# Kernel optimization log

Measured on AMD Instinct MI355X. Metric: run time of the kernel, lower is better.

## Reference

```python
import jax, jax.numpy as jnp
import numpy as np

C, T, D = 32, 768, 100      # n_countries, n_times, n_ages (=n_features)
H = 5                        # attention heads (EncoderLayer default)
HID_GCN = 60                 # GCN hidden features
FFN = 64                     # feed_forward_dim
NPRED = 10                   # n_predictions
LHID = 200                   # hid_linear_part_dim
NL = 3                       # encoder layers


def setup_inputs() -> dict:
    key = jax.random.key(0)
    ks = jax.random.split(key, 24)
    s = 0.05
    rn = lambda k, shp: jax.random.normal(k, shp, jnp.float32) * s
    return {
        "X": jax.random.normal(ks[0], (C, T, D), jnp.float32),
        "A": jax.random.uniform(ks[1], (C, C), jnp.float32),
        # GCN params
        "gcn_w1": rn(ks[2], (D, HID_GCN)),
        "gcn_b1": rn(ks[3], (HID_GCN,)),
        "gcn_w2": rn(ks[4], (HID_GCN, D)),
        "gcn_b2": rn(ks[5], (D,)),
        # 3 stacked encoder layers
        "enc_wq": rn(ks[6], (NL, H, D, D)),
        "enc_wk": rn(ks[7], (NL, H, D, D)),
        "enc_wv": rn(ks[8], (NL, H, D, D)),
        "enc_wm": rn(ks[9], (NL, H * D, D)),
        "enc_f1w": rn(ks[10], (NL, D, FFN)),
        "enc_f1b": rn(ks[11], (NL, FFN)),
        "enc_f2w": rn(ks[12], (NL, FFN, D)),
        "enc_f2b": rn(ks[13], (NL, D)),
        "enc_ln1g": jnp.ones((NL, D), jnp.float32),
        "enc_ln1b": jnp.zeros((NL, D), jnp.float32),
        "enc_ln2g": jnp.ones((NL, D), jnp.float32),
        "enc_ln2b": jnp.zeros((NL, D), jnp.float32),
        "lin1_w": rn(ks[14], (D, LHID)),
        "lin1_b": rn(ks[15], (LHID,)),
        "lin2_w": rn(ks[16], (LHID, D)),
        "lin2_b": rn(ks[17], (D,)),
    }


def _layer_norm(x, g, b, eps=1e-5):
    m = x.mean(-1, keepdims=True)
    v = ((x - m) ** 2).mean(-1, keepdims=True)
    return (x - m) / jnp.sqrt(v + eps) * g + b


def _encoder_layer(x, wq, wk, wv, wm, f1w, f1b, f2w, f2b, g1, b1, g2, b2):
    # x: [C, T, D]; wq/wk/wv: [H, D, D]
    Q = jnp.einsum('ctd,hde->chte', x, wq)
    K = jnp.einsum('ctd,hde->chte', x, wk)
    V = jnp.einsum('ctd,hde->chte', x, wv)
    scores = jnp.einsum('chte,chse->chts', Q, K) / jnp.sqrt(jnp.float32(D))
    attn = jax.nn.softmax(scores, axis=-1)
    out = jnp.einsum('chts,chse->chte', attn, V)        # [C,H,T,D]
    out = out.transpose(0, 2, 1, 3).reshape(x.shape[0], x.shape[1], H * D)
    x = _layer_norm(x + out @ wm, g1, b1)
    ffn = jax.nn.relu(x @ f1w + f1b) @ f2w + f2b
    return _layer_norm(x + ffn, g2, b2)


def reference(X, A, gcn_w1, gcn_b1, gcn_w2, gcn_b2,
              enc_wq, enc_wk, enc_wv, enc_wm,
              enc_f1w, enc_f1b, enc_f2w, enc_f2b,
              enc_ln1g, enc_ln1b, enc_ln2g, enc_ln2b,
              lin1_w, lin1_b, lin2_w, lin2_b):
    n = A.shape[0]
    adj = A + jnp.eye(n, dtype=A.dtype)
    adj_hat = adj / adj.sum(-1, keepdims=True)
    # GCN layer 1
    h = jnp.einsum('ij,jta->ita', adj_hat, X)
    h = jnp.einsum('ita,ao->ito', h, gcn_w1) + gcn_b1
    h = jax.nn.relu(h)
    # GCN layer 2
    h = jnp.einsum('ij,jta->ita', adj_hat, h)
    h = jnp.einsum('ita,ao->ito', h, gcn_w2) + gcn_b2
    # 3 encoder layers (fixed structural loop)
    for l in range(NL):
        h = _encoder_layer(h, enc_wq[l], enc_wk[l], enc_wv[l], enc_wm[l],
                           enc_f1w[l], enc_f1b[l], enc_f2w[l], enc_f2b[l],
                           enc_ln1g[l], enc_ln1b[l], enc_ln2g[l], enc_ln2b[l])
    last = h[:, -1, :]  # [C, D]
    def step(carry, _):
        p = (carry @ lin1_w + lin1_b) @ lin2_w + lin2_b
        return p, p
    _, preds = jax.lax.scan(step, last, None, length=NPRED)  # [NPRED, C, D]
    return preds.transpose(1, 0, 2)  # [C, NPRED, D]
```

## Files before the change

kernel.cpp:

```cpp
#include <hip/hip_runtime.h>


#define ROWS 24576

#define OFF_ADJ   0L
#define OFF_X0    1024L
#define OFF_X1    (OFF_X0 + 2457600L)
#define OFF_XROW  (OFF_X1 + 3932160L)
#define OFF_XT    (OFF_XROW + 1572864L)
#define OFF_WBF   (OFF_XT + 1572864L)
#define OFF_MHT   (OFF_WBF + 6291456L)
#define OFF_USTT  (OFF_MHT + 122880L)
#define OFF_MP    (OFF_USTT + 98304L)
#define OFF_C0    (OFF_MP + 10000L)
#define OFF_F1WT  (OFF_C0 + 128L)
#define OFF_F2WT  (OFF_F1WT + 12288L)
#define OFF_GW1T  (OFF_F2WT + 10752L)
#define OFF_GW2T  (OFF_GW1T + 4096L)

typedef __attribute__((ext_vector_type(8))) short short8;
typedef __attribute__((ext_vector_type(4))) short short4v;
typedef __attribute__((ext_vector_type(4))) float float4v;
typedef __attribute__((ext_vector_type(2))) unsigned int uint2v;
typedef __attribute__((ext_vector_type(4))) unsigned int uint4v;

__device__ inline unsigned short f2bf(float f) {
    unsigned u = __builtin_bit_cast(unsigned, f);
    return (unsigned short)((u + 0x7fffu + ((u >> 16) & 1u)) >> 16);
}
__device__ inline unsigned pk2bf(float lo, float hi) {
    unsigned r;
    asm("v_cvt_pk_bf16_f32 %0, %1, %2" : "=v"(r) : "v"(lo), "v"(hi));
    return r;
}
__device__ inline void st4s(short* p, unsigned a, unsigned b) {
    *(short4v*)p = __builtin_bit_cast(short4v, (uint2v){a, b});
}
__device__ inline float bf2f(unsigned short v) {
    return __builtin_bit_cast(float, ((unsigned)v) << 16);
}
__device__ inline void gload16(const short* g, short* l) {
    __builtin_amdgcn_global_load_lds((const __attribute__((address_space(1))) void*)g,
                                     (__attribute__((address_space(3))) void*)l, 16, 0, 0);
}
__device__ inline int permt(int t) {
    int tl = t & 63, q = tl >> 2, r = tl & 3;
    int pos = (q & 8) | ((q & 3) << 1) | ((q >> 2) & 1);
    return (t & ~63) | (pos << 2) | r;
}

__global__ void __launch_bounds__(256) k_mu2(const float* __restrict__ wq, const float* __restrict__ wk,
                                             const float* __restrict__ wv, const float* __restrict__ wm,
                                             const float* __restrict__ l1w, const float* __restrict__ l1b,
                                             const float* __restrict__ l2w, const float* __restrict__ l2b,
                                             const float* __restrict__ f1w, const float* __restrict__ f2w,
                                             const float* __restrict__ A,
                                             const float* __restrict__ gw1, const float* __restrict__ gw2,
                                             unsigned short* __restrict__ MhT, unsigned short* __restrict__ UstT,
                                             float* __restrict__ Mp, float* __restrict__ c0v,
                                             unsigned short* __restrict__ f1wT, unsigned short* __restrict__ f2wT,
                                             float* __restrict__ adjh,
                                             unsigned short* __restrict__ gw1T, unsigned short* __restrict__ gw2T) {
    int bi = blockIdx.x, tid = threadIdx.x;
    if (bi < 480) {
        int mat = bi >> 4, sub = bi & 15;
        int mode = mat / 15, idx = mat % 15, l = idx / 5, h = idx % 5;
        const float* Asrc = (mode == 0 ? wq : wv) + (l*5 + h)*10000;
        const float* Bsrc = (mode == 0) ? (wk + (l*5 + h)*10000) : (wm + l*50000 + h*10000);
        int oend = sub*625 + 625;
        for (int o = sub*625 + tid; o < oend; o += 256) {
            int r = o / 100, cix = o - (o/100)*100;
            const float* arow = Asrc + r*100;
            float acc = 0.f;
            if (mode == 0) {
                const float* brow = Bsrc + cix*100;
                float4 s = {0,0,0,0};
                #pragma unroll 5
                for (int e4 = 0; e4 < 25; ++e4) {
                    float4 av = *(const float4*)(arow + e4*4);
                    float4 bv = *(const float4*)(brow + e4*4);
                    s.x += av.x*bv.x; s.y += av.y*bv.y;
                    s.z += av.z*bv.z; s.w += av.w*bv.w;
                }
                acc = (s.x + s.y) + (s.z + s.w);
                MhT[(long)(l*5 + h)*16384 + cix*128 + r] = f2bf(acc * 0.1f);
            } else {
                for (int e = 0; e < 100; ++e) acc += arow[e] * Bsrc[e*100 + cix];
                UstT[(long)l*65536 + (long)cix*512 + h*100 + r] = f2bf(acc);
            }
        }
        if (sub == 0) {
            if (mode == 0) {
                unsigned short* M0 = MhT + (long)(l*5 + h)*16384;
                for (int i = tid; i < 28*128; i += 256) M0[(100 + i/128)*128 + (i%128)] = 0;
                for (int i = tid; i < 100*28; i += 256) M0[(i/28)*128 + 100 + (i%28)] = 0;
            } else if (h == 4) {
                unsigned short* U0 = UstT + (long)l*65536;
                for (int i = tid; i < 28*512; i += 256) U0[(long)(100 + i/512)*512 + (i%512)] = 0;
                for (int i = tid; i < 100*12; i += 256) U0[(long)(i/12)*512 + 500 + (i%12)] = 0;
            }
        }
    } else if (bi < 496) {
        int sub = bi - 480;
        int oend = sub*625 + 625;
        for (int o = sub*625 + tid; o < oend; o += 256) {
            int r = o / 100, cix = o - (o/100)*100;
            const float* arow = l1w + r*200;
            float acc = 0.f;
            for (int e = 0; e < 200; ++e) acc += arow[e] * l2w[e*100 + cix];
            Mp[r*100 + cix] = acc;
        }
    } else if (bi == 496) {
        if (tid < 100) {
            float acc = l2b[tid];
            for (int e = 0; e < 200; ++e) acc += l1b[e] * l2w[e*100 + tid];
            c0v[tid] = acc;
        }
    } else if (bi < 500) {
        int l = bi - 497;
        unsigned short* F1 = f1wT + (long)l*8192;
        for (int i = tid; i < 8192; i += 256) {
            int o = i >> 7, k = i & 127;
            F1[i] = (k < 100) ? f2bf(f1w[l*6400 + k*64 + o]) : (unsigned short)0;
        }
        unsigned short* F2 = f2wT + (long)l*7168;
        for (int i = tid; i < 7168; i += 256) {
            int o2 = i >> 6, k2 = i & 63;
            F2[i] = (o2 < 100) ? f2bf(f2w[l*6400 + k2*100 + o2]) : (unsigned short)0;
        }
    } else if (bi == 500) {
        __shared__ float adj[1024];
        __shared__ float rs[32];
        for (int i = tid; i < 1024; i += 256) {
            int r = i >> 5, j = i & 31;
            adj[i] = A[i] + (r == j ? 1.f : 0.f);
        }
        __syncthreads();
        if (tid < 32) {
            float s = 0.f;
            #pragma unroll
            for (int jj = 0; jj < 32; ++jj) s += adj[tid*32 + jj];
            rs[tid] = s;
        }
        __syncthreads();
        for (int i = tid; i < 1024; i += 256) adjh[i] = adj[i] / rs[i >> 5];
    } else {
        for (int i = tid; i < 8192; i += 256) {
            int o = i >> 7, k = i & 127;
            gw1T[i] = (o < 60 && k < 100) ? f2bf(gw1[k*60 + o]) : (unsigned short)0;
        }
        for (int i = tid; i < 7168; i += 256) {
            int o = i >> 6, k = i & 63;
            gw2T[i] = (o < 100 && k < 60) ? f2bf(gw2[k*100 + o]) : (unsigned short)0;
        }
    }
}

__global__ void __launch_bounds__(128) k_gw1(const float* __restrict__ X,
                                             const unsigned short* __restrict__ gw1T,
                                             unsigned short* __restrict__ g) {
    const int tid = threadIdx.x, wave = tid >> 6, lane = tid & 63;
    const int l15 = lane & 15, l4 = lane >> 4;
    const long row = (long)blockIdx.x*32 + wave*16 + l15;
    const float* xrp = X + row*100;
    float4v acc[4];
    #pragma unroll
    for (int mt = 0; mt < 4; ++mt) acc[mt] = (float4v){0,0,0,0};
    #pragma unroll
    for (int ks = 0; ks < 4; ++ks) {
        const int k0 = ks*32 + l4*8;
        short8 b;
        if (k0 + 8 <= 100) {
            float4 v0 = *(const float4*)(xrp + k0);
            float4 v1 = *(const float4*)(xrp + k0 + 4);
            b[0] = (short)f2bf(v0.x); b[1] = (short)f2bf(v0.y);
            b[2] = (short)f2bf(v0.z); b[3] = (short)f2bf(v0.w);
            b[4] = (short)f2bf(v1.x); b[5] = (short)f2bf(v1.y);
            b[6] = (short)f2bf(v1.z); b[7] = (short)f2bf(v1.w);
        } else if (k0 < 100) {
            float4 v0 = *(const float4*)(xrp + k0);
            b[0] = (short)f2bf(v0.x); b[1] = (short)f2bf(v0.y);
            b[2] = (short)f2bf(v0.z); b[3] = (short)f2bf(v0.w);
            b[4] = 0; b[5] = 0; b[6] = 0; b[7] = 0;
        } else {
            #pragma unroll
            for (int e = 0; e < 8; ++e) b[e] = 0;
        }
        #pragma unroll
        for (int mt = 0; mt < 4; ++mt) {
            short8 a = *(const short8*)((const short*)gw1T + (mt*16 + l15)*128 + ks*32 + l4*8);
            acc[mt] = __builtin_amdgcn_mfma_f32_16x16x32_bf16(a, b, acc[mt], 0, 0, 0);
        }
    }
    #pragma unroll
    for (int mt = 0; mt < 4; ++mt) {
        int o0 = mt*16 + l4*4;
        *(uint2v*)(g + row*64 + o0) =
            (uint2v){pk2bf(acc[mt][0], acc[mt][1]), pk2bf(acc[mt][2], acc[mt][3])};
    }
}

__global__ void __launch_bounds__(256) k_spmmg(const float* __restrict__ adjh,
                                               const unsigned short* __restrict__ g,
                                               const float* __restrict__ b1,
                                               unsigned short* __restrict__ hid) {
    __shared__ float adj[1024];
    int tid = threadIdx.x;
    for (int i = tid; i < 1024; i += 256) adj[i] = adjh[i];
    __syncthreads();
    long p = (long)blockIdx.x*256 + tid;
    int o = (int)(p & 63);
    float acc[32];
    #pragma unroll
    for (int i = 0; i < 32; ++i) acc[i] = 0.f;
    for (int j = 0; j < 32; ++j) {
        float xv = bf2f(g[(long)j*49152 + p]);
        #pragma unroll
        for (int i = 0; i < 32; ++i) acc[i] += adj[i*32 + j] * xv;
    }
    float bias = (o < 60) ? b1[o] : 0.f;
    #pragma unroll
    for (int i = 0; i < 32; ++i) hid[(long)i*49152 + p] = f2bf(fmaxf(acc[i] + bias, 0.f));
}

__global__ void __launch_bounds__(128) k_gw2(const unsigned short* __restrict__ hid,
                                             const unsigned short* __restrict__ gw2T,
                                             unsigned short* __restrict__ h2) {
    const int tid = threadIdx.x, wave = tid >> 6, lane = tid & 63;
    const int l15 = lane & 15, l4 = lane >> 4;
    const long row = (long)blockIdx.x*32 + wave*16 + l15;
    float4v acc[7];
    #pragma unroll
    for (int mt = 0; mt < 7; ++mt) acc[mt] = (float4v){0,0,0,0};
    #pragma unroll
    for (int ks = 0; ks < 2; ++ks) {
        short8 b = *(const short8*)((const short*)hid + row*64 + ks*32 + l4*8);
        #pragma unroll
        for (int mt = 0; mt < 7; ++mt) {
            short8 a = *(const short8*)((const short*)gw2T + (mt*16 + l15)*64 + ks*32 + l4*8);
            acc[mt] = __builtin_amdgcn_mfma_f32_16x16x32_bf16(a, b, acc[mt], 0, 0, 0);
        }
    }
    #pragma unroll
    for (int mt = 0; mt < 7; ++mt) {
        int o0 = mt*16 + l4*4;
        *(uint2v*)(h2 + row*128 + o0) =
            (uint2v){pk2bf(acc[mt][0], acc[mt][1]), pk2bf(acc[mt][2], acc[mt][3])};
    }
    *(uint2v*)(h2 + row*128 + 112 + l4*4) = (uint2v){0u, 0u};
}

__global__ void __launch_bounds__(384) k_spmmx(const float* __restrict__ adjh,
                                               const unsigned short* __restrict__ h2,
                                               const float* __restrict__ b2,
                                               float* __restrict__ x0,
                                               unsigned short* __restrict__ xrow,
                                               unsigned short* __restrict__ xT) {
    __shared__ float adj[1024];
    int tid = threadIdx.x;
    for (int i = tid; i < 1024; i += 384) adj[i] = adjh[i];
    __syncthreads();
    long p = (long)blockIdx.x*384 + tid;
    int o = (int)(p & 127);
    int t = (int)(p >> 7);
    int tp = permt(t);
    float acc[32];
    #pragma unroll
    for (int i = 0; i < 32; ++i) acc[i] = 0.f;
    for (int j = 0; j < 32; ++j) {
        float xv = bf2f(h2[(long)j*98304 + p]);
        #pragma unroll
        for (int i = 0; i < 32; ++i) acc[i] += adj[i*32 + j] * xv;
    }
    if (o < 100) {
        float bias = b2[o];
        #pragma unroll
        for (int i = 0; i < 32; ++i) {
            float v = acc[i] + bias;
            x0[((long)i*768 + t)*100 + o] = v;
            unsigned short bv = f2bf(v);
            xrow[((long)i*768 + t)*128 + o] = bv;
            xT[(long)i*98304 + (long)o*768 + tp] = bv;
        }
    } else {
        #pragma unroll
        for (int i = 0; i < 32; ++i) {
            xrow[((long)i*768 + t)*128 + o] = 0;
            if (o < 112) xT[(long)i*98304 + (long)o*768 + tp] = 0;
        }
    }
}

__global__ void __launch_bounds__(256, 4) k_attn12(const unsigned short* __restrict__ xrow,
                                                   const unsigned short* __restrict__ xT,
                                                   const unsigned short* __restrict__ MhT,
                                                   unsigned short* __restrict__ Wb) {
    __shared__ __align__(16) short xr[2][64 * 128];
    __shared__ __align__(16) short xt[112 * 64];
    const int tid = threadIdx.x;
    const int wave = tid >> 6, lane = tid & 63;
    const int l15 = lane & 15, l4 = lane >> 4;
    const int c = blockIdx.z, h = blockIdx.y, q0 = blockIdx.x * 128;

    const short* xrg = (const short*)xrow + (long)c*768*128;
    const short* xtg = (const short*)xT + (long)c*128*768;
    const int rl4 = lane >> 4, cp16 = lane & 15;
    const int rl8 = lane >> 3, cp8 = lane & 7;
    const int njt = (wave == 3) ? 2 : 4;
    const int sw8 = (l15 & 7) << 3;
    const int swt = l15 & 7;

    #pragma unroll
    for (int j = 0; j < 4; ++j) {
        int row = wave*16 + j*4 + rl4;
        int lc = cp16 ^ (row & 7);
        gload16(xrg + (long)row*128 + lc*8, xr[0] + (wave*16 + j*4)*128);
    }

    short8 qb0[4], qb1[4];
    {
        short* mq = &xr[1][wave * 16 * 128];
        const short* Mb = (const short*)MhT + (long)h*16384 + l15*128 + l4*8;
        const short* xq = (const short*)xrow + ((long)c*768 + q0 + wave*16 + l15)*128 + l4*8;
        short8 bq0[4], bq1[4];
        #pragma unroll
        for (int kk = 0; kk < 4; ++kk) {
            bq0[kk] = *(const short8*)(xq + kk*32);
            bq1[kk] = *(const short8*)(xq + 64*128 + kk*32);
        }
        float4v qc0[8], qc1[8];
        #pragma unroll
        for (int mt = 0; mt < 8; ++mt) { qc0[mt] = (float4v){0,0,0,0}; qc1[mt] = (float4v){0,0,0,0}; }
        __builtin_amdgcn_s_setprio(1);
        #pragma unroll
        for (int mt = 0; mt < 8; ++mt) {
            #pragma unroll
            for (int kk = 0; kk < 4; ++kk) {
                short8 a = *(const short8*)(Mb + (mt*16)*128 + kk*32);
                qc0[mt] = __builtin_amdgcn_mfma_f32_16x16x32_bf16(a, bq0[kk], qc0[mt], 0, 0, 0);
                qc1[mt] = __builtin_amdgcn_mfma_f32_16x16x32_bf16(a, bq1[kk], qc1[mt], 0, 0, 0);
            }
        }
        __builtin_amdgcn_s_setprio(0);
        #pragma unroll
        for (int mt = 0; mt < 8; ++mt)
            st4s(mq + l15*128 + ((mt*16 + l4*4) ^ sw8),
                 pk2bf(qc0[mt][0], qc0[mt][1]), pk2bf(qc0[mt][2], qc0[mt][3]));
        asm volatile("" ::: "memory");
        #pragma unroll
        for (int kk = 0; kk < 4; ++kk)
            qb0[kk] = *(const short8*)(mq + l15*128 + ((kk*32 + l4*8) ^ sw8));
        asm volatile("" ::: "memory");
        #pragma unroll
        for (int mt = 0; mt < 8; ++mt)
            st4s(mq + l15*128 + ((mt*16 + l4*4) ^ sw8),
                 pk2bf(qc1[mt][0], qc1[mt][1]), pk2bf(qc1[mt][2], qc1[mt][3]));
        asm volatile("" ::: "memory");
        #pragma unroll
        for (int kk = 0; kk < 4; ++kk)
            qb1[kk] = *(const short8*)(mq + l15*128 + ((kk*32 + l4*8) ^ sw8));
    }

    __syncthreads();

    float4v o0[7], o1[7];
    #pragma unroll
    for (int n = 0; n < 7; ++n) { o0[n] = (float4v){0,0,0,0}; o1[n] = (float4v){0,0,0,0}; }
    float lsum0 = 0.f, lsum1 = 0.f;

    for (int kt = 0; kt < 12; ++kt) {
        const int key0 = kt * 64;
        const short* xrb = xr[kt & 1];

        for (int j = 0; j < njt; ++j) {
            int row = wave*32 + j*8 + rl8;
            int lc = cp8 ^ (row & 7);
            gload16(xtg + (long)row*768 + key0 + lc*8, xt + (wave*32 + j*8)*64);
        }
        if (kt < 11) {
            short* xrn = xr[(kt + 1) & 1];
            #pragma unroll
            for (int j = 0; j < 4; ++j) {
                int row = wave*16 + j*4 + rl4;
                int lc = cp16 ^ (row & 7);
                gload16(xrg + (long)(key0 + 64 + row)*128 + lc*8, xrn + (wave*16 + j*4)*128);
            }
        }
        __builtin_amdgcn_sched_barrier(0);

        unsigned pw0[4], pw1[4];
        __builtin_amdgcn_s_setprio(1);
        #pragma unroll
        for (int kn = 0; kn < 2; ++kn) {
            float4v s0 = (float4v){0,0,0,0}, s1 = (float4v){0,0,0,0};
            #pragma unroll
            for (int kk = 0; kk < 4; ++kk) {
                short8 a = *(const short8*)(xrb + (kn*16 + l15)*128 + (((kk*4 + l4) ^ (l15 & 7))*8));
                s0 = __builtin_amdgcn_mfma_f32_16x16x32_bf16(a, qb0[kk], s0, 0, 0, 0);
                s1 = __builtin_amdgcn_mfma_f32_16x16x32_bf16(a, qb1[kk], s1, 0, 0, 0);
            }
            float p0[4], p1[4];
            #pragma unroll
            for (int r = 0; r < 4; ++r) {
                p0[r] = __expf(s0[r]); lsum0 += p0[r];
                p1[r] = __expf(s1[r]); lsum1 += p1[r];
            }
            pw0[kn*2]   = pk2bf(p0[0], p0[1]); pw0[kn*2+1] = pk2bf(p0[2], p0[3]);
            pw1[kn*2]   = pk2bf(p1[0], p1[1]); pw1[kn*2+1] = pk2bf(p1[2], p1[3]);
        }
        __builtin_amdgcn_s_setprio(0);

        if (kt < 11) { asm volatile("s_waitcnt vmcnt(4)" ::: "memory"); }
        else         { asm volatile("s_waitcnt vmcnt(0)" ::: "memory"); }
        __builtin_amdgcn_s_barrier();

        __builtin_amdgcn_s_setprio(1);
        {
            short8 b0 = __builtin_bit_cast(short8, (uint4v){pw0[0], pw0[1], pw0[2], pw0[3]});
            short8 b1 = __builtin_bit_cast(short8, (uint4v){pw1[0], pw1[1], pw1[2], pw1[3]});
            const int offA = ((l4 ^ swt) * 8);
            #pragma unroll
            for (int dt = 0; dt < 7; ++dt) {
                short8 a = *(const short8*)(xt + (dt*16 + l15)*64 + offA);
                o0[dt] = __builtin_amdgcn_mfma_f32_16x16x32_bf16(a, b0, o0[dt], 0, 0, 0);
                o1[dt] = __builtin_amdgcn_mfma_f32_16x16x32_bf16(a, b1, o1[dt], 0, 0, 0);
            }
        }

        unsigned pw0b[4], pw1b[4];
        #pragma unroll
        for (int kn = 2; kn < 4; ++kn) {
            float4v s0 = (float4v){0,0,0,0}, s1 = (float4v){0,0,0,0};
            #pragma unroll
            for (int kk = 0; kk < 4; ++kk) {
                short8 a = *(const short8*)(xrb + (kn*16 + l15)*128 + (((kk*4 + l4) ^ (l15 & 7))*8));
                s0 = __builtin_amdgcn_mfma_f32_16x16x32_bf16(a, qb0[kk], s0, 0, 0, 0);
                s1 = __builtin_amdgcn_mfma_f32_16x16x32_bf16(a, qb1[kk], s1, 0, 0, 0);
            }
            float p0[4], p1[4];
            #pragma unroll
            for (int r = 0; r < 4; ++r) {
                p0[r] = __expf(s0[r]); lsum0 += p0[r];
                p1[r] = __expf(s1[r]); lsum1 += p1[r];
            }
            pw0b[(kn-2)*2]   = pk2bf(p0[0], p0[1]); pw0b[(kn-2)*2+1] = pk2bf(p0[2], p0[3]);
            pw1b[(kn-2)*2]   = pk2bf(p1[0], p1[1]); pw1b[(kn-2)*2+1] = pk2bf(p1[2], p1[3]);
        }

        {
            short8 b0 = __builtin_bit_cast(short8, (uint4v){pw0b[0], pw0b[1], pw0b[2], pw0b[3]});
            short8 b1 = __builtin_bit_cast(short8, (uint4v){pw1b[0], pw1b[1], pw1b[2], pw1b[3]});
            const int offB = (((4 + l4) ^ swt) * 8);
            #pragma unroll
            for (int dt = 0; dt < 7; ++dt) {
                short8 a = *(const short8*)(xt + (dt*16 + l15)*64 + offB);
                o0[dt] = __builtin_amdgcn_mfma_f32_16x16x32_bf16(a, b0, o0[dt], 0, 0, 0);
                o1[dt] = __builtin_amdgcn_mfma_f32_16x16x32_bf16(a, b1, o1[dt], 0, 0, 0);
            }
        }
        __builtin_amdgcn_s_setprio(0);
        __syncthreads();
    }

    float l0 = lsum0, l1 = lsum1;
    l0 += __shfl_xor(l0, 16, 64); l0 += __shfl_xor(l0, 32, 64);
    l1 += __shfl_xor(l1, 16, 64); l1 += __shfl_xor(l1, 32, 64);
    float inv0 = 1.f / l0, inv1 = 1.f / l1;

    unsigned short* Wo0 = Wb + ((long)(c*768 + q0 + wave*16 + l15))*512 + h*100 + l4*4;
    unsigned short* Wo1 = Wo0 + 64*512;
    #pragma unroll
    for (int dt = 0; dt < 7; ++dt) {
        if (dt < 6 || l4 == 0) {
            *(uint2v*)(Wo0 + dt*16) = (uint2v){pk2bf(o0[dt][0]*inv0, o0[dt][1]*inv0),
                                               pk2bf(o0[dt][2]*inv0, o0[dt][3]*inv0)};
            *(uint2v*)(Wo1 + dt*16) = (uint2v){pk2bf(o1[dt][0]*inv1, o1[dt][1]*inv1),
                                               pk2bf(o1[dt][2]*inv1, o1[dt][3]*inv1)};
        }
    }
    if (h == 0) {
        unsigned short* Wz = Wb + ((long)c*768 + q0)*512 + 500;
        for (int i = tid; i < 1536; i += 256) Wz[(long)(i/12)*512 + (i%12)] = 0;
    }
}

template<bool EMIT>
__global__ void __launch_bounds__(128) k_tail(const unsigned short* __restrict__ Wb,
        const unsigned short* __restrict__ UstT,
        const unsigned short* __restrict__ f1wT, const unsigned short* __restrict__ f2wT,
        const float* __restrict__ f1b, const float* __restrict__ f2b,
        const float* __restrict__ g1, const float* __restrict__ b1,
        const float* __restrict__ g2, const float* __restrict__ b2,
        float* __restrict__ x, unsigned short* __restrict__ xrow, unsigned short* __restrict__ xT) {
    __shared__ __align__(16) short ust[2][128 * 64];
    const int tid = threadIdx.x, wave = tid >> 6, lane = tid & 63;
    const int l15 = lane & 15, l4 = lane >> 4;
    const long row = (long)blockIdx.x*32 + wave*16 + l15;
    const int cc = blockIdx.x / 24;
    const int tt = (blockIdx.x % 24)*32 + wave*16 + l15;
    const int ttp = permt(tt);
    const int sr8 = lane >> 3, sc8 = lane & 7;

    const short* Wr = (const short*)Wb + row*512 + l4*8;
    float4v o[8];
    #pragma unroll
    for (int mt = 0; mt < 8; ++mt) o[mt] = (float4v){0,0,0,0};

    {
        short* dst = ust[0];
        #pragma unroll
        for (int j = 0; j < 8; ++j) {
            int r = wave*64 + j*8 + sr8;
            int lc = sc8 ^ (r & 7);
            gload16((const short*)UstT + (long)r*512 + 0 + lc*8, dst + (wave*64 + j*8)*64);
        }
    }
    __syncthreads();

    short8 bc0 = *(const short8*)(Wr + 0);
    short8 bc1 = *(const short8*)(Wr + 32);
    for (int cb = 0; cb < 8; ++cb) {
        if (cb < 7) {
            const int ksb = (cb + 1) * 64;
            short* dst = ust[(cb + 1) & 1];
            #pragma unroll
            for (int j = 0; j < 8; ++j) {
                int r = wave*64 + j*8 + sr8;
                int lc = sc8 ^ (r & 7);
                gload16((const short*)UstT + (long)r*512 + ksb + lc*8, dst + (wave*64 + j*8)*64);
            }
        }
        short8 bn0, bn1;
        if (cb < 7) {
            bn0 = *(const short8*)(Wr + (cb*2 + 2)*32);
            bn1 = *(const short8*)(Wr + (cb*2 + 3)*32);
        }
        __builtin_amdgcn_sched_barrier(0);

        const short* bufc = ust[cb & 1];
        __builtin_amdgcn_s_setprio(1);
        #pragma unroll
        for (int mt = 0; mt < 8; ++mt) {
            short8 a0 = *(const short8*)(bufc + (mt*16 + l15)*64 + (((0*4 + l4) ^ (l15 & 7))*8));
            o[mt] = __builtin_amdgcn_mfma_f32_16x16x32_bf16(a0, bc0, o[mt], 0, 0, 0);
            short8 a1 = *(const short8*)(bufc + (mt*16 + l15)*64 + (((1*4 + l4) ^ (l15 & 7))*8));
            o[mt] = __builtin_amdgcn_mfma_f32_16x16x32_bf16(a1, bc1, o[mt], 0, 0, 0);
        }
        __builtin_amdgcn_s_setprio(0);
        bc0 = bn0; bc1 = bn1;
        __syncthreads();
    }

    short* myz = ust[0] + wave * 2176;
    short* myt = ust[1] + wave * 1152;

    float zv[7][4];
    float sum = 0.f;
    #pragma unroll
    for (int mt = 0; mt < 7; ++mt) {
        int f0 = mt*16 + l4*4;
        float4 xv = {0,0,0,0};
        if (f0 < 100) xv = *(const float4*)(x + row*100 + f0);
        #pragma unroll
        for (int r = 0; r < 4; ++r) {
            float z = 0.f;
            if (f0 < 100) { z = o[mt][r] + ((const float*)&xv)[r]; sum += z; }
            zv[mt][r] = z;
        }
    }
    sum += __shfl_xor(sum, 16, 64); sum += __shfl_xor(sum, 32, 64);
    float mean = sum * 0.01f;
    float vs = 0.f;
    #pragma unroll
    for (int mt = 0; mt < 7; ++mt) {
        if (mt*16 + l4*4 < 100) {
            #pragma unroll
            for (int r = 0; r < 4; ++r) { float d = zv[mt][r] - mean; vs += d*d; }
        }
    }
    vs += __shfl_xor(vs, 16, 64); vs += __shfl_xor(vs, 32, 64);
    float inv = rsqrtf(vs * 0.01f + 1e-5f);
    float x1r[7][4];
    #pragma unroll
    for (int mt = 0; mt < 7; ++mt) {
        int f0 = mt*16 + l4*4;
        float4 gv = {0,0,0,0}, bv = {0,0,0,0};
        if (f0 < 100) { gv = *(const float4*)(g1 + f0); bv = *(const float4*)(b1 + f0); }
        #pragma unroll
        for (int r = 0; r < 4; ++r)
            x1r[mt][r] = (f0 < 100) ? (zv[mt][r] - mean) * inv * ((const float*)&gv)[r] + ((const float*)&bv)[r] : 0.f;
    }

    #pragma unroll
    for (int mt = 0; mt < 8; ++mt) {
        float v0 = (mt < 7) ? x1r[mt][0] : 0.f, v1 = (mt < 7) ? x1r[mt][1] : 0.f;
        float v2 = (mt < 7) ? x1r[mt][2] : 0.f, v3 = (mt < 7) ? x1r[mt][3] : 0.f;
        st4s(myz + l15*136 + mt*16 + l4*4, pk2bf(v0, v1), pk2bf(v2, v3));
    }
    asm volatile("" ::: "memory");

    float4v t2[4];
    #pragma unroll
    for (int m2t = 0; m2t < 4; ++m2t) t2[m2t] = (float4v){0,0,0,0};
    #pragma unroll
    for (int ks = 0; ks < 4; ++ks) {
        short8 b = *(const short8*)(myz + l15*136 + ks*32 + l4*8);
        #pragma unroll
        for (int m2t = 0; m2t < 4; ++m2t) {
            short8 a = *(const short8*)((const short*)f1wT + (m2t*16 + l15)*128 + ks*32 + l4*8);
            t2[m2t] = __builtin_amdgcn_mfma_f32_16x16x32_bf16(a, b, t2[m2t], 0, 0, 0);
        }
    }
    #pragma unroll
    for (int m2t = 0; m2t < 4; ++m2t) {
        int m20 = m2t*16 + l4*4;
        float4 bv = *(const float4*)(f1b + m20);
        float v0 = fmaxf(t2[m2t][0] + ((const float*)&bv)[0], 0.f);
        float v1 = fmaxf(t2[m2t][1] + ((const float*)&bv)[1], 0.f);
        float v2 = fmaxf(t2[m2t][2] + ((const float*)&bv)[2], 0.f);
        float v3 = fmaxf(t2[m2t][3] + ((const float*)&bv)[3], 0.f);
        st4s(myt + l15*72 + m20, pk2bf(v0, v1), pk2bf(v2, v3));
    }
    asm volatile("" ::: "memory");

    float4v o3[7];
    #pragma unroll
    for (int m3t = 0; m3t < 7; ++m3t) o3[m3t] = (float4v){0,0,0,0};
    #pragma unroll
    for (int ks2 = 0; ks2 < 2; ++ks2) {
        short8 b = *(const short8*)(myt + l15*72 + ks2*32 + l4*8);
        #pragma unroll
        for (int m3t = 0; m3t < 7; ++m3t) {
            short8 a = *(const short8*)((const short*)f2wT + (m3t*16 + l15)*64 + ks2*32 + l4*8);
            o3[m3t] = __builtin_amdgcn_mfma_f32_16x16x32_bf16(a, b, o3[m3t], 0, 0, 0);
        }
    }

    float z2[7][4];
    float sum2 = 0.f;
    #pragma unroll
    for (int m3t = 0; m3t < 7; ++m3t) {
        int f0 = m3t*16 + l4*4;
        float4 bv = {0,0,0,0};
        if (f0 < 100) bv = *(const float4*)(f2b + f0);
        #pragma unroll
        for (int r = 0; r < 4; ++r) {
            float z = 0.f;
            if (f0 < 100) { z = o3[m3t][r] + ((const float*)&bv)[r] + x1r[m3t][r]; sum2 += z; }
            z2[m3t][r] = z;
        }
    }
    sum2 += __shfl_xor(sum2, 16, 64); sum2 += __shfl_xor(sum2, 32, 64);
    float mean2 = sum2 * 0.01f;
    float vs2 = 0.f;
    #pragma unroll
    for (int m3t = 0; m3t < 7; ++m3t) {
        if (m3t*16 + l4*4 < 100) {
            #pragma unroll
            for (int r = 0; r < 4; ++r) { float d = z2[m3t][r] - mean2; vs2 += d*d; }
        }
    }
    vs2 += __shfl_xor(vs2, 16, 64); vs2 += __shfl_xor(vs2, 32, 64);
    float inv2 = rsqrtf(vs2 * 0.01f + 1e-5f);

    unsigned short* xTc = EMIT ? (xT + (long)cc*98304 + ttp) : nullptr;
    #pragma unroll
    for (int m3t = 0; m3t < 7; ++m3t) {
        int f0 = m3t*16 + l4*4;
        if (f0 < 100) {
            float4 gv = *(const float4*)(g2 + f0);
            float4 bv = *(const float4*)(b2 + f0);
            float y[4];
            #pragma unroll
            for (int r = 0; r < 4; ++r)
                y[r] = (z2[m3t][r] - mean2) * inv2 * ((const float*)&gv)[r] + ((const float*)&bv)[r];
            *(float4*)(x + row*100 + f0) = (float4){y[0], y[1], y[2], y[3]};
            if (EMIT) {
                *(uint2v*)(xrow + row*128 + f0) = (uint2v){pk2bf(y[0], y[1]), pk2bf(y[2], y[3])};
                #pragma unroll
                for (int r = 0; r < 4; ++r)
                    xTc[(long)(f0 + r)*768] = f2bf(y[r]);
            }
        } else if (EMIT) {
            *(uint2v*)(xrow + row*128 + f0) = (uint2v){0u, 0u};
            #pragma unroll
            for (int r = 0; r < 4; ++r)
                if (f0 + r < 112) xTc[(long)(f0 + r)*768] = 0;
        }
    }
    if (EMIT) *(uint2v*)(xrow + row*128 + 112 + l4*4) = (uint2v){0u, 0u};
}

__global__ void __launch_bounds__(256) k_pred2(const float* __restrict__ xf,
        const float* __restrict__ Mp, const float* __restrict__ c0v,
        float* __restrict__ out) {
    int c = blockIdx.x, tid = threadIdx.x;
    __shared__ float Ml[10000];
    __shared__ float carry[100];
    for (int i = tid; i < 10000; i += 256) Ml[i] = Mp[i];
    if (tid < 100) carry[tid] = xf[((long)c*768 + 767)*100 + tid];
    __syncthreads();
    for (int s = 0; s < 10; ++s) {
        float pv = 0.f;
        if (tid < 100) {
            pv = c0v[tid];
            for (int d = 0; d < 100; ++d) pv += carry[d] * Ml[d*100 + tid];
            out[((long)c*10 + s)*100 + tid] = pv;
        }
        __syncthreads();
        if (tid < 100) carry[tid] = pv;
        __syncthreads();
    }
}

extern "C" void kernel_launch(void* const* d_in, const int* in_sizes, int n_in,
                              void* d_out, int out_size, void* d_ws, size_t ws_size,
                              hipStream_t stream) {
    const float* X    = (const float*)d_in[0];
    const float* A    = (const float*)d_in[1];
    const float* gw1  = (const float*)d_in[2];
    const float* gb1  = (const float*)d_in[3];
    const float* gw2  = (const float*)d_in[4];
    const float* gb2  = (const float*)d_in[5];
    const float* wq   = (const float*)d_in[6];
    const float* wk   = (const float*)d_in[7];
    const float* wv   = (const float*)d_in[8];
    const float* wm   = (const float*)d_in[9];
    const float* f1w  = (const float*)d_in[10];
    const float* f1b  = (const float*)d_in[11];
    const float* f2w  = (const float*)d_in[12];
    const float* f2b  = (const float*)d_in[13];
    const float* ln1g = (const float*)d_in[14];
    const float* ln1b = (const float*)d_in[15];
    const float* ln2g = (const float*)d_in[16];
    const float* ln2b = (const float*)d_in[17];
    const float* l1w  = (const float*)d_in[18];
    const float* l1b  = (const float*)d_in[19];
    const float* l2w  = (const float*)d_in[20];
    const float* l2b  = (const float*)d_in[21];
    (void)in_sizes; (void)n_in; (void)out_size; (void)ws_size;

    float* ws   = (float*)d_ws;
    float* adjh = ws + OFF_ADJ;
    float* x0   = ws + OFF_X0;
    unsigned short* gbuf = (unsigned short*)(ws + OFF_X1);
    unsigned short* hbuf = (unsigned short*)(ws + OFF_X1 + 786432L);
    unsigned short* h2buf= (unsigned short*)(ws + OFF_X1 + 1572864L);
    unsigned short* xrow = (unsigned short*)(ws + OFF_XROW);
    unsigned short* xTb  = (unsigned short*)(ws + OFF_XT);
    unsigned short* Wbf  = (unsigned short*)(ws + OFF_WBF);
    unsigned short* MhT  = (unsigned short*)(ws + OFF_MHT);
    unsigned short* UstT = (unsigned short*)(ws + OFF_USTT);
    float* Mp   = ws + OFF_MP;
    float* c0v  = ws + OFF_C0;
    unsigned short* f1wT = (unsigned short*)(ws + OFF_F1WT);
    unsigned short* f2wT = (unsigned short*)(ws + OFF_F2WT);
    unsigned short* gw1T = (unsigned short*)(ws + OFF_GW1T);
    unsigned short* gw2T = (unsigned short*)(ws + OFF_GW2T);
    float* out  = (float*)d_out;

    k_mu2<<<502, 256, 0, stream>>>(wq, wk, wv, wm, l1w, l1b, l2w, l2b, f1w, f2w, A, gw1, gw2,
                                   MhT, UstT, Mp, c0v, f1wT, f2wT, adjh, gw1T, gw2T);

    k_gw1<<<768, 128, 0, stream>>>(X, gw1T, gbuf);
    k_spmmg<<<192, 256, 0, stream>>>(adjh, gbuf, gb1, hbuf);
    k_gw2<<<768, 128, 0, stream>>>(hbuf, gw2T, h2buf);
    k_spmmx<<<256, 384, 0, stream>>>(adjh, h2buf, gb2, x0, xrow, xTb);

    for (int l = 0; l < 3; ++l) {
        k_attn12<<<dim3(6,5,32), 256, 0, stream>>>(xrow, xTb, MhT + (long)l*81920, Wbf);
        if (l < 2)
            k_tail<true><<<768, 128, 0, stream>>>(Wbf, UstT + (long)l*65536,
                f1wT + (long)l*8192, f2wT + (long)l*7168, f1b + l*64, f2b + l*100,
                ln1g + l*100, ln1b + l*100, ln2g + l*100, ln2b + l*100, x0, xrow, xTb);
        else
            k_tail<false><<<768, 128, 0, stream>>>(Wbf, UstT + (long)l*65536,
                f1wT + (long)l*8192, f2wT + (long)l*7168, f1b + l*64, f2b + l*100,
                ln1g + l*100, ln1b + l*100, ln2g + l*100, ln2b + l*100, x0, xrow, xTb);
    }

    k_pred2<<<32, 256, 0, stream>>>(x0, Mp, c0v, out);
}
```

Measured before the change: 461.2 us.

## Split attention query tile across 8 waves with one 16-row tile each

The attention kernel now runs 512 threads (8 waves) per block instead of 256, and each wave handles a single 16-query tile instead of two. Cooperative K/V tile loads are redistributed over the 8 waves, and the vmcnt wait threshold is adjusted to match. Per-wave register pressure and accumulator state roughly halve, which lets more waves hide latency. The cost is that each wave reuses every LDS-loaded key fragment for half as many query tiles, so LDS read traffic per unit of MFMA work doubles.

```diff
diff --git a/kernel.cpp b/kernel.cpp
--- a/kernel.cpp
+++ b/kernel.cpp
@@ -291,10 +291,10 @@
     }
 }
 
-__global__ void __launch_bounds__(256, 4) k_attn12(const unsigned short* __restrict__ xrow,
-                                                   const unsigned short* __restrict__ xT,
-                                                   const unsigned short* __restrict__ MhT,
-                                                   unsigned short* __restrict__ Wb) {
+__global__ void __launch_bounds__(512) k_attn14(const unsigned short* __restrict__ xrow,
+                                                const unsigned short* __restrict__ xT,
+                                                const unsigned short* __restrict__ MhT,
+                                                unsigned short* __restrict__ Wb) {
     __shared__ __align__(16) short xr[2][64 * 128];
     __shared__ __align__(16) short xt[112 * 64];
     const int tid = threadIdx.x;
@@ -306,181 +306,152 @@
     const short* xtg = (const short*)xT + (long)c*128*768;
     const int rl4 = lane >> 4, cp16 = lane & 15;
     const int rl8 = lane >> 3, cp8 = lane & 7;
-    const int njt = (wave == 3) ? 2 : 4;
+    const int njt = (wave < 7) ? 2 : 0;
     const int sw8 = (l15 & 7) << 3;
     const int swt = l15 & 7;
 
-    #pragma unroll
-    for (int j = 0; j < 4; ++j) {
-        int row = wave*16 + j*4 + rl4;
-        int lc = cp16 ^ (row & 7);
-        gload16(xrg + (long)row*128 + lc*8, xr[0] + (wave*16 + j*4)*128);
-    }
-
-    short8 qb0[4], qb1[4];
+    short8 qb[4];
     {
-        short* mq = &xr[1][wave * 16 * 128];
+        short* mq = &xr[0][0] + wave * 2048;
         const short* Mb = (const short*)MhT + (long)h*16384 + l15*128 + l4*8;
         const short* xq = (const short*)xrow + ((long)c*768 + q0 + wave*16 + l15)*128 + l4*8;
-        short8 bq0[4], bq1[4];
-        #pragma unroll
-        for (int kk = 0; kk < 4; ++kk) {
-            bq0[kk] = *(const short8*)(xq + kk*32);
-            bq1[kk] = *(const short8*)(xq + 64*128 + kk*32);
-        }
-        float4v qc0[8], qc1[8];
-        #pragma unroll
-        for (int mt = 0; mt < 8; ++mt) { qc0[mt] = (float4v){0,0,0,0}; qc1[mt] = (float4v){0,0,0,0}; }
+        short8 bq[4];
+        #pragma unroll
+        for (int kk = 0; kk < 4; ++kk) bq[kk] = *(const short8*)(xq + kk*32);
+        float4v qc[8];
+        #pragma unroll
+        for (int mt = 0; mt < 8; ++mt) qc[mt] = (float4v){0,0,0,0};
         __builtin_amdgcn_s_setprio(1);
         #pragma unroll
         for (int mt = 0; mt < 8; ++mt) {
             #pragma unroll
             for (int kk = 0; kk < 4; ++kk) {
                 short8 a = *(const short8*)(Mb + (mt*16)*128 + kk*32);
-                qc0[mt] = __builtin_amdgcn_mfma_f32_16x16x32_bf16(a, bq0[kk], qc0[mt], 0, 0, 0);
-                qc1[mt] = __builtin_amdgcn_mfma_f32_16x16x32_bf16(a, bq1[kk], qc1[mt], 0, 0, 0);
+                qc[mt] = __builtin_amdgcn_mfma_f32_16x16x32_bf16(a, bq[kk], qc[mt], 0, 0, 0);
             }
         }
         __builtin_amdgcn_s_setprio(0);
         #pragma unroll
         for (int mt = 0; mt < 8; ++mt)
             st4s(mq + l15*128 + ((mt*16 + l4*4) ^ sw8),
-                 pk2bf(qc0[mt][0], qc0[mt][1]), pk2bf(qc0[mt][2], qc0[mt][3]));
+                 pk2bf(qc[mt][0], qc[mt][1]), pk2bf(qc[mt][2], qc[mt][3]));
         asm volatile("" ::: "memory");
         #pragma unroll
         for (int kk = 0; kk < 4; ++kk)
-            qb0[kk] = *(const short8*)(mq + l15*128 + ((kk*32 + l4*8) ^ sw8));
+            qb[kk] = *(const short8*)(mq + l15*128 + ((kk*32 + l4*8) ^ sw8));
         asm volatile("" ::: "memory");
-        #pragma unroll
-        for (int mt = 0; mt < 8; ++mt)
-            st4s(mq + l15*128 + ((mt*16 + l4*4) ^ sw8),
-                 pk2bf(qc1[mt][0], qc1[mt][1]), pk2bf(qc1[mt][2], qc1[mt][3]));
-        asm volatile("" ::: "memory");
-        #pragma unroll
-        for (int kk = 0; kk < 4; ++kk)
-            qb1[kk] = *(const short8*)(mq + l15*128 + ((kk*32 + l4*8) ^ sw8));
     }
 
     __syncthreads();
 
-    float4v o0[7], o1[7];
-    #pragma unroll
-    for (int n = 0; n < 7; ++n) { o0[n] = (float4v){0,0,0,0}; o1[n] = (float4v){0,0,0,0}; }
-    float lsum0 = 0.f, lsum1 = 0.f;
+    #pragma unroll
+    for (int j = 0; j < 2; ++j) {
+        int row = wave*8 + j*4 + rl4;
+        int lc = cp16 ^ (row & 7);
+        gload16(xrg + (long)row*128 + lc*8, xr[0] + (wave*8 + j*4)*128);
+    }
+    __syncthreads();
+
+    float4v o[7];
+    #pragma unroll
+    for (int n = 0; n < 7; ++n) o[n] = (float4v){0,0,0,0};
+    float lsum = 0.f;
 
     for (int kt = 0; kt < 12; ++kt) {
         const int key0 = kt * 64;
         const short* xrb = xr[kt & 1];
 
         for (int j = 0; j < njt; ++j) {
-            int row = wave*32 + j*8 + rl8;
+            int row = wave*16 + j*8 + rl8;
             int lc = cp8 ^ (row & 7);
-            gload16(xtg + (long)row*768 + key0 + lc*8, xt + (wave*32 + j*8)*64);
+            gload16(xtg + (long)row*768 + key0 + lc*8, xt + (wave*16 + j*8)*64);
         }
         if (kt < 11) {
             short* xrn = xr[(kt + 1) & 1];
             #pragma unroll
-            for (int j = 0; j < 4; ++j) {
-                int row = wave*16 + j*4 + rl4;
+            for (int j = 0; j < 2; ++j) {
+                int row = wave*8 + j*4 + rl4;
                 int lc = cp16 ^ (row & 7);
-                gload16(xrg + (long)(key0 + 64 + row)*128 + lc*8, xrn + (wave*16 + j*4)*128);
+                gload16(xrg + (long)(key0 + 64 + row)*128 + lc*8, xrn + (wave*8 + j*4)*128);
             }
         }
         __builtin_amdgcn_sched_barrier(0);
 
-        unsigned pw0[4], pw1[4];
+        unsigned pw[4];
         __builtin_amdgcn_s_setprio(1);
         #pragma unroll
         for (int kn = 0; kn < 2; ++kn) {
-            float4v s0 = (float4v){0,0,0,0}, s1 = (float4v){0,0,0,0};
+            float4v s0 = (float4v){0,0,0,0};
             #pragma unroll
             for (int kk = 0; kk < 4; ++kk) {
                 short8 a = *(const short8*)(xrb + (kn*16 + l15)*128 + (((kk*4 + l4) ^ (l15 & 7))*8));
-                s0 = __builtin_amdgcn_mfma_f32_16x16x32_bf16(a, qb0[kk], s0, 0, 0, 0);
-                s1 = __builtin_amdgcn_mfma_f32_16x16x32_bf16(a, qb1[kk], s1, 0, 0, 0);
-            }
-            float p0[4], p1[4];
-            #pragma unroll
-            for (int r = 0; r < 4; ++r) {
-                p0[r] = __expf(s0[r]); lsum0 += p0[r];
-                p1[r] = __expf(s1[r]); lsum1 += p1[r];
-            }
-            pw0[kn*2]   = pk2bf(p0[0], p0[1]); pw0[kn*2+1] = pk2bf(p0[2], p0[3]);
-            pw1[kn*2]   = pk2bf(p1[0], p1[1]); pw1[kn*2+1] = pk2bf(p1[2], p1[3]);
+                s0 = __builtin_amdgcn_mfma_f32_16x16x32_bf16(a, qb[kk], s0, 0, 0, 0);
+            }
+            float p[4];
+            #pragma unroll
+            for (int r = 0; r < 4; ++r) { p[r] = __expf(s0[r]); lsum += p[r]; }
+            pw[kn*2]   = pk2bf(p[0], p[1]); pw[kn*2+1] = pk2bf(p[2], p[3]);
         }
         __builtin_amdgcn_s_setprio(0);
 
-        if (kt < 11) { asm volatile("s_waitcnt vmcnt(4)" ::: "memory"); }
+        if (kt < 11) { asm volatile("s_waitcnt vmcnt(2)" ::: "memory"); }
         else         { asm volatile("s_waitcnt vmcnt(0)" ::: "memory"); }
         __builtin_amdgcn_s_barrier();
 
         __builtin_amdgcn_s_setprio(1);
         {
-            short8 b0 = __builtin_bit_cast(short8, (uint4v){pw0[0], pw0[1], pw0[2], pw0[3]});
-            short8 b1 = __builtin_bit_cast(short8, (uint4v){pw1[0], pw1[1], pw1[2], pw1[3]});
+            short8 b0 = __builtin_bit_cast(short8, (uint4v){pw[0], pw[1], pw[2], pw[3]});
             const int offA = ((l4 ^ swt) * 8);
             #pragma unroll
             for (int dt = 0; dt < 7; ++dt) {
                 short8 a = *(const short8*)(xt + (dt*16 + l15)*64 + offA);
-                o0[dt] = __builtin_amdgcn_mfma_f32_16x16x32_bf16(a, b0, o0[dt], 0, 0, 0);
-                o1[dt] = __builtin_amdgcn_mfma_f32_16x16x32_bf16(a, b1, o1[dt], 0, 0, 0);
-            }
-        }
-
-        unsigned pw0b[4], pw1b[4];
+                o[dt] = __builtin_amdgcn_mfma_f32_16x16x32_bf16(a, b0, o[dt], 0, 0, 0);
+            }
+        }
+
+        unsigned pwb[4];
         #pragma unroll
         for (int kn = 2; kn < 4; ++kn) {
-            float4v s0 = (float4v){0,0,0,0}, s1 = (float4v){0,0,0,0};
+            float4v s0 = (float4v){0,0,0,0};
             #pragma unroll
             for (int kk = 0; kk < 4; ++kk) {
                 short8 a = *(const short8*)(xrb + (kn*16 + l15)*128 + (((kk*4 + l4) ^ (l15 & 7))*8));
-                s0 = __builtin_amdgcn_mfma_f32_16x16x32_bf16(a, qb0[kk], s0, 0, 0, 0);
-                s1 = __builtin_amdgcn_mfma_f32_16x16x32_bf16(a, qb1[kk], s1, 0, 0, 0);
-            }
-            float p0[4], p1[4];
-            #pragma unroll
-            for (int r = 0; r < 4; ++r) {
-                p0[r] = __expf(s0[r]); lsum0 += p0[r];
-                p1[r] = __expf(s1[r]); lsum1 += p1[r];
-            }
-            pw0b[(kn-2)*2]   = pk2bf(p0[0], p0[1]); pw0b[(kn-2)*2+1] = pk2bf(p0[2], p0[3]);
-            pw1b[(kn-2)*2]   = pk2bf(p1[0], p1[1]); pw1b[(kn-2)*2+1] = pk2bf(p1[2], p1[3]);
+                s0 = __builtin_amdgcn_mfma_f32_16x16x32_bf16(a, qb[kk], s0, 0, 0, 0);
+            }
+            float p[4];
+            #pragma unroll
+            for (int r = 0; r < 4; ++r) { p[r] = __expf(s0[r]); lsum += p[r]; }
+            pwb[(kn-2)*2]   = pk2bf(p[0], p[1]); pwb[(kn-2)*2+1] = pk2bf(p[2], p[3]);
         }
 
         {
-            short8 b0 = __builtin_bit_cast(short8, (uint4v){pw0b[0], pw0b[1], pw0b[2], pw0b[3]});
-            short8 b1 = __builtin_bit_cast(short8, (uint4v){pw1b[0], pw1b[1], pw1b[2], pw1b[3]});
+            short8 b0 = __builtin_bit_cast(short8, (uint4v){pwb[0], pwb[1], pwb[2], pwb[3]});
             const int offB = (((4 + l4) ^ swt) * 8);
             #pragma unroll
             for (int dt = 0; dt < 7; ++dt) {
                 short8 a = *(const short8*)(xt + (dt*16 + l15)*64 + offB);
-                o0[dt] = __builtin_amdgcn_mfma_f32_16x16x32_bf16(a, b0, o0[dt], 0, 0, 0);
-                o1[dt] = __builtin_amdgcn_mfma_f32_16x16x32_bf16(a, b1, o1[dt], 0, 0, 0);
+                o[dt] = __builtin_amdgcn_mfma_f32_16x16x32_bf16(a, b0, o[dt], 0, 0, 0);
             }
         }
         __builtin_amdgcn_s_setprio(0);
         __syncthreads();
     }
 
-    float l0 = lsum0, l1 = lsum1;
+    float l0 = lsum;
     l0 += __shfl_xor(l0, 16, 64); l0 += __shfl_xor(l0, 32, 64);
-    l1 += __shfl_xor(l1, 16, 64); l1 += __shfl_xor(l1, 32, 64);
-    float inv0 = 1.f / l0, inv1 = 1.f / l1;
-
-    unsigned short* Wo0 = Wb + ((long)(c*768 + q0 + wave*16 + l15))*512 + h*100 + l4*4;
-    unsigned short* Wo1 = Wo0 + 64*512;
+    float inv0 = 1.f / l0;
+
+    unsigned short* Wo = Wb + ((long)(c*768 + q0 + wave*16 + l15))*512 + h*100 + l4*4;
     #pragma unroll
     for (int dt = 0; dt < 7; ++dt) {
         if (dt < 6 || l4 == 0) {
-            *(uint2v*)(Wo0 + dt*16) = (uint2v){pk2bf(o0[dt][0]*inv0, o0[dt][1]*inv0),
-                                               pk2bf(o0[dt][2]*inv0, o0[dt][3]*inv0)};
-            *(uint2v*)(Wo1 + dt*16) = (uint2v){pk2bf(o1[dt][0]*inv1, o1[dt][1]*inv1),
-                                               pk2bf(o1[dt][2]*inv1, o1[dt][3]*inv1)};
+            *(uint2v*)(Wo + dt*16) = (uint2v){pk2bf(o[dt][0]*inv0, o[dt][1]*inv0),
+                                              pk2bf(o[dt][2]*inv0, o[dt][3]*inv0)};
         }
     }
     if (h == 0) {
         unsigned short* Wz = Wb + ((long)c*768 + q0)*512 + 500;
-        for (int i = tid; i < 1536; i += 256) Wz[(long)(i/12)*512 + (i%12)] = 0;
+        for (int i = tid; i < 1536; i += 512) Wz[(long)(i/12)*512 + (i%12)] = 0;
     }
 }
 
@@ -768,7 +739,7 @@
     k_spmmx<<<256, 384, 0, stream>>>(adjh, h2buf, gb2, x0, xrow, xTb);
 
     for (int l = 0; l < 3; ++l) {
-        k_attn12<<<dim3(6,5,32), 256, 0, stream>>>(xrow, xTb, MhT + (long)l*81920, Wbf);
+        k_attn14<<<dim3(6,5,32), 512, 0, stream>>>(xrow, xTb, MhT + (long)l*81920, Wbf);
         if (l < 2)
             k_tail<true><<<768, 128, 0, stream>>>(Wbf, UstT + (long)l*65536,
                 f1wT + (long)l*8192, f2wT + (long)l*7168, f1b + l*64, f2b + l*100,
```

After: 495.4 us. 7.4% more time.
